# Performance work log

Measured on AMD Instinct MI355X. Metric: run time of the kernel, lower is better.

## Reference

```python
import jax, jax.numpy as jnp
import numpy as np
from math import sqrt

NUM_HEADS = 8
HIDDEN = 768
ATTN_DIM = HIDDEN // NUM_HEADS  # 96
NEG = -1e10


def setup_inputs() -> dict:
    key = jax.random.key(0)
    ks = jax.random.split(key, 6)
    b, s, dim = 8, 1024, 768
    scale = 1.0 / sqrt(dim)
    return {
        "span_embeddings": jax.random.normal(ks[0], (b, s, dim), dtype=jnp.float32),
        "span_tags": jax.random.randint(ks[1], (b, s), 0, 5),
        "w_weight": jax.random.normal(ks[2], (1, dim), dtype=jnp.float32) * scale,
        "w_q": jax.random.normal(ks[3], (HIDDEN, dim), dtype=jnp.float32) * scale,
        "w_k": jax.random.normal(ks[4], (HIDDEN, dim), dtype=jnp.float32) * scale,
        "w_v": jax.random.normal(ks[5], (HIDDEN, dim), dtype=jnp.float32) * scale,
    }


def reference(span_embeddings, span_tags, w_weight, w_q, w_k, w_v):
    b, s, _ = span_embeddings.shape
    pad = span_tags == 0  # [b, s]

    # additive span attention weights: Linear(dim -> 1), mask padded, softmax over seq
    attn_weights = span_embeddings @ w_weight.T  # [b, s, 1]
    attn_weights = jnp.where(pad[:, :, None], NEG, attn_weights)
    attn_weights = jax.nn.softmax(attn_weights, axis=1)

    # NOTE: original views hidden as (attn_dim, num_heads) in that order
    qs = (span_embeddings @ w_q.T).reshape(b, s, ATTN_DIM, NUM_HEADS)
    ks = (span_embeddings @ w_k.T).reshape(b, s, ATTN_DIM, NUM_HEADS)
    vs = (span_embeddings @ w_v.T).reshape(b, s, ATTN_DIM, NUM_HEADS)

    rel = jnp.einsum('bqdh,bkdh->bqkh', qs, ks) / sqrt(ATTN_DIM)  # [b,q,k,h]
    # original masks along query axis (relevance_weights[span_tags.eq(0)] = NEG)
    rel = jnp.where(pad[:, :, None, None], NEG, rel)
    # original softmax(dim=-1) -> over the HEADS axis (faithful quirk)
    rel = jax.nn.softmax(rel, axis=-1)

    span_value = jnp.einsum('bqkh,bkdh->bqdh', rel, vs).reshape(b, s, HIDDEN)
    weighted_value = jnp.sum(attn_weights * span_value, axis=1)  # [b, hidden]
    return weighted_value
```

## Files before the change

### kernel.cpp

```cpp
#include <hip/hip_runtime.h>
#include <hip/hip_bf16.h>
#include <math.h>

#define NEGV (-1e10f)

typedef __attribute__((ext_vector_type(8))) short bf16x8;
typedef __attribute__((ext_vector_type(4))) float f32x4;
typedef __attribute__((ext_vector_type(16))) float f32x16;

static __device__ __forceinline__ unsigned short f2bf(float f) {
  unsigned int u = __builtin_bit_cast(unsigned int, f);
  unsigned int r = (u + 0x7fffu + ((u >> 16) & 1u)) >> 16;
  return (unsigned short)r;
}
static __device__ __forceinline__ float bf2f(unsigned short v) {
  return __builtin_bit_cast(float, (unsigned int)v << 16);
}

#define GLD16(g, l)                                                   \
  __builtin_amdgcn_global_load_lds(                                   \
      (const __attribute__((address_space(1))) void*)(g),             \
      (__attribute__((address_space(3))) void*)(l), 16, 0, 0)

__global__ __launch_bounds__(256) void cast_inputs(
    const float* __restrict__ emb, const int* __restrict__ tags,
    const float* __restrict__ ww, const float* __restrict__ wq,
    const float* __restrict__ wk, const float* __restrict__ wv,
    unsigned short* __restrict__ embbf, float* __restrict__ logits,
    unsigned short* __restrict__ wbf) {
  int bx = blockIdx.x;
  if (bx < 2048) {
    int w = threadIdx.x >> 6, lane = threadIdx.x & 63;
    int row = bx * 4 + w;
    const float4* src = (const float4*)(emb + (size_t)row * 768);
    const float4* wsrc = (const float4*)ww;
    ushort4* dst = (ushort4*)(embbf + (size_t)row * 768);
    float d = 0.f;
#pragma unroll
    for (int j = 0; j < 3; j++) {
      int idx = lane + 64 * j;
      float4 v = src[idx];
      float4 wv = wsrc[idx];
      d += v.x * wv.x + v.y * wv.y + v.z * wv.z + v.w * wv.w;
      ushort4 o;
      o.x = f2bf(v.x); o.y = f2bf(v.y); o.z = f2bf(v.z); o.w = f2bf(v.w);
      dst[idx] = o;
    }
#pragma unroll
    for (int off = 32; off; off >>= 1) d += __shfl_xor(d, off);
    if (lane == 0) logits[row] = (tags[row] == 0) ? NEGV : d;
  } else {
    int g = bx - 2048;
    int z = g / 576;
    int idx = (g - z * 576) * 256 + threadIdx.x;
    const float* src = (z == 0) ? wq : (z == 1) ? wk : wv;
    float4 v = ((const float4*)src)[idx];
    ushort4 o;
    o.x = f2bf(v.x); o.y = f2bf(v.y); o.z = f2bf(v.z); o.w = f2bf(v.w);
    if (z == 2) {
      ((ushort4*)(wbf + (size_t)z * 589824))[idx] = o;
    } else {
      int f = idx / 192;
      int col4 = idx - f * 192;
      int h = f & 7, dg = f >> 3;
      int tt = dg >> 4, ddl = dg & 15;
      int wn = ddl >> 3, cb = (ddl >> 2) & 1, j = ddl & 3;
      int orow = tt * 128 + wn * 64 + j * 16 + cb * 8 + h;
      ((ushort4*)(wbf + (size_t)z * 589824))[orow * 192 + col4] = o;
    }
  }
}

__global__ __launch_bounds__(256) void softmax_aw(
    const float* __restrict__ logits, float* __restrict__ aw) {
  __shared__ float red[4];
  int b = blockIdx.x, t = threadIdx.x;
  const float* L = logits + b * 1024;
  float x0 = L[t], x1 = L[t + 256], x2 = L[t + 512], x3 = L[t + 768];
  float m = fmaxf(fmaxf(x0, x1), fmaxf(x2, x3));
#pragma unroll
  for (int off = 32; off; off >>= 1) m = fmaxf(m, __shfl_xor(m, off));
  if ((t & 63) == 0) red[t >> 6] = m;
  __syncthreads();
  m = fmaxf(fmaxf(red[0], red[1]), fmaxf(red[2], red[3]));
  float e0 = __expf(x0 - m), e1 = __expf(x1 - m), e2 = __expf(x2 - m),
        e3 = __expf(x3 - m);
  float s = e0 + e1 + e2 + e3;
#pragma unroll
  for (int off = 32; off; off >>= 1) s += __shfl_xor(s, off);
  __syncthreads();
  if ((t & 63) == 0) red[t >> 6] = s;
  __syncthreads();
  float inv = 1.0f / (red[0] + red[1] + red[2] + red[3]);
  float* A = aw + b * 1024;
  A[t] = e0 * inv; A[t + 256] = e1 * inv;
  A[t + 512] = e2 * inv; A[t + 768] = e3 * inv;
}

__global__ __launch_bounds__(256) void qkv_gemm(
    const unsigned short* __restrict__ A, const unsigned short* __restrict__ Wbf,
    unsigned short* __restrict__ Qf, unsigned short* __restrict__ Kf,
    unsigned short* __restrict__ Vbf) {
  __shared__ __align__(16) unsigned short sm[17408];
  unsigned short* As = sm;
  unsigned short* Bs = sm + 8192;
  int z = blockIdx.z;
  const unsigned short* B = Wbf + (size_t)z * 589824;
  int mb = blockIdx.x * 128, nb = blockIdx.y * 128;
  int tid = threadIdx.x;
  int w = tid >> 6, lane = tid & 63;
  int wm = w >> 1, wn = w & 1;
  int c = lane & 15, quad = lane >> 4;
  int lrow = lane >> 2;
  int lcol = ((lane & 3) ^ (lrow & 3)) * 8;
  const unsigned short* Ag = A + (size_t)(mb + w * 32 + lrow) * 768 + lcol;
  const unsigned short* Bg = B + (size_t)(nb + w * 32 + lrow) * 768 + lcol;
  int woff = w * 1024;

#define PREFETCH(buf, kb)                                              \
  do {                                                                 \
    GLD16(Ag + (kb), As + (buf) * 4096 + woff);                        \
    GLD16(Ag + (kb) + 16 * 768, As + (buf) * 4096 + woff + 512);       \
    GLD16(Bg + (kb), Bs + (buf) * 4096 + woff);                        \
    GLD16(Bg + (kb) + 16 * 768, Bs + (buf) * 4096 + woff + 512);       \
  } while (0)

  f32x4 acc[4][4];
#pragma unroll
  for (int i = 0; i < 4; i++)
#pragma unroll
    for (int j = 0; j < 4; j++) acc[i][j] = 0;

  PREFETCH(0, 0);
  for (int it = 0; it < 24; it++) {
    __syncthreads();
    if (it + 1 < 24) PREFETCH((it + 1) & 1, (it + 1) * 32);
    const unsigned short* Ab = As + (it & 1) * 4096;
    const unsigned short* Bb = Bs + (it & 1) * 4096;
    int sw = (quad ^ (c & 3)) * 8;
    bf16x8 af[4], bfr[4];
#pragma unroll
    for (int i = 0; i < 4; i++)
      af[i] = *(const bf16x8*)&Ab[(wm * 64 + i * 16 + c) * 32 + sw];
#pragma unroll
    for (int j = 0; j < 4; j++)
      bfr[j] = *(const bf16x8*)&Bb[(wn * 64 + j * 16 + c) * 32 + sw];
#pragma unroll
    for (int i = 0; i < 4; i++)
#pragma unroll
      for (int j = 0; j < 4; j++)
        acc[i][j] = __builtin_amdgcn_mfma_f32_16x16x32_bf16(af[i], bfr[j],
                                                            acc[i][j], 0, 0, 0);
  }
  __syncthreads();

  if (z == 2) {
#pragma unroll
    for (int i = 0; i < 4; i++)
#pragma unroll
      for (int j = 0; j < 4; j++)
#pragma unroll
        for (int r = 0; r < 4; r++) {
          int rl = wm * 64 + i * 16 + quad * 4 + r;
          int cl = wn * 64 + j * 16 + c;
          sm[rl * 136 + cl] = f2bf(acc[i][j][r]);
        }
    __syncthreads();
#pragma unroll
    for (int it2 = 0; it2 < 8; it2++) {
      int g2 = it2 * 256 + tid;
      int rl = g2 >> 4;
      int cu = (g2 & 15) * 8;
      bf16x8 vdat = *(const bf16x8*)&sm[rl * 136 + cu];
      *(bf16x8*)&Vbf[(size_t)(mb + rl) * 768 + nb + cu] = vdat;
    }
  } else {
    unsigned short* O = (z == 0) ? Qf : Kf;
#pragma unroll
    for (int i = 0; i < 4; i++) {
#pragma unroll
      for (int r = 0; r < 4; r++) {
        int qlr = wm * 64 + i * 16 + quad * 4 + r;
        int chunkL = (qlr >> 5) * 8 + (c & 7);
        int lane32 = (qlr & 31) + wn * 32;
        ushort4 pk;
        pk.x = f2bf(acc[i][0][r]);
        pk.y = f2bf(acc[i][1][r]);
        pk.z = f2bf(acc[i][2][r]);
        pk.w = f2bf(acc[i][3][r]);
        *(ushort4*)&sm[chunkL * 520 + lane32 * 8 + 4 * (c >> 3)] = pk;
      }
    }
    __syncthreads();
    int bq = mb >> 10;
    int qt32g0 = (mb & 1023) >> 5;
    int tt = blockIdx.y;
#pragma unroll
    for (int it2 = 0; it2 < 8; it2++) {
      int g = it2 * 256 + tid;
      int chunkL = g >> 6;
      int off = (g & 63) * 8;
      bf16x8 vdat = *(const bf16x8*)&sm[chunkL * 520 + off];
      int qt32 = qt32g0 + (chunkL >> 3), h = chunkL & 7;
      size_t dst = ((((size_t)(bq * 32 + qt32) * 8 + h) * 6 + tt) << 9) + off;
      *(bf16x8*)&O[dst] = vdat;
    }
  }
#undef PREFETCH
}

__global__ __launch_bounds__(256) void attn(
    const unsigned short* __restrict__ Qf, const unsigned short* __restrict__ Kf,
    const float* __restrict__ aw, float* __restrict__ Ptp) {
  __shared__ float pbuf[1024];
  int id = blockIdx.x;
  int b = id & 7, qb = (id >> 3) & 15, kb = id >> 7;
  int tid = threadIdx.x, w = tid >> 6, lane = tid & 63;
  int wq = w >> 1, wk = w & 1;
  const unsigned short* Qb =
      Qf + ((size_t)(b * 32 + qb * 2 + wq) * 48) * 512 + (size_t)lane * 8;
  const unsigned short* Kb =
      Kf + ((size_t)(b * 32 + kb * 2 + wk) * 48) * 512 + (size_t)lane * 8;

  f32x16 acc[8];
#pragma unroll
  for (int h = 0; h < 8; h++) acc[h] = 0;
#pragma unroll
  for (int h = 0; h < 8; h++) {
#pragma unroll
    for (int t = 0; t < 6; t++) {
      bf16x8 a = *(const bf16x8*)(Qb + (size_t)(h * 6 + t) * 512);
      bf16x8 bb = *(const bf16x8*)(Kb + (size_t)(h * 6 + t) * 512);
      acc[h] = __builtin_amdgcn_mfma_f32_32x32x16_bf16(a, bb, acc[h], 0, 0, 0);
    }
  }

  float awv[16];
#pragma unroll
  for (int reg = 0; reg < 16; reg++) {
    int row = (reg & 3) + 8 * (reg >> 2) + 4 * (lane >> 5);
    awv[reg] = aw[b * 1024 + qb * 64 + wq * 32 + row];
  }
  float partial[8];
#pragma unroll
  for (int h = 0; h < 8; h++) partial[h] = 0.f;
  const float C2 = 0.10206207261596577f * 1.4426950408889634f;
#pragma unroll
  for (int reg = 0; reg < 16; reg++) {
    float v[8];
    float ssum = 0.f;
#pragma unroll
    for (int h = 0; h < 8; h++) {
      float e = exp2f(acc[h][reg] * C2);
      v[h] = e;
      ssum += e;
    }
    float g = awv[reg] * __builtin_amdgcn_rcpf(ssum);
#pragma unroll
    for (int h = 0; h < 8; h++) partial[h] += v[h] * g;
  }
#pragma unroll
  for (int h = 0; h < 8; h++) {
    float v = partial[h];
    v += __shfl_xor(v, 32);
    partial[h] = v;
  }
  if (lane < 32) {
#pragma unroll
    for (int h = 0; h < 8; h++) pbuf[w * 256 + lane * 8 + h] = partial[h];
  }
  __syncthreads();
#pragma unroll
  for (int wk2 = 0; wk2 < 2; wk2++) {
    float s = pbuf[wk2 * 256 + tid] + pbuf[(2 + wk2) * 256 + tid];
    int kcol = tid >> 3, h = tid & 7;
    Ptp[(((size_t)qb * 8 + b) * 1024 + kb * 64 + wk2 * 32 + kcol) * 8 + h] = s;
  }
}

__global__ __launch_bounds__(256) void finalize(
    const float* __restrict__ Ptp, const unsigned short* __restrict__ Vbf,
    float* __restrict__ out) {
  __shared__ float ps[256];
  int kc = blockIdx.x, b = blockIdx.y;
  int t = threadIdx.x;
  {
    int k = kc * 32 + (t >> 3), h = t & 7;
    float s = 0.f;
#pragma unroll
    for (int qc = 0; qc < 16; qc++)
      s += Ptp[(((size_t)qc * 8 + b) * 1024 + k) * 8 + h];
    ps[t] = s;
  }
  __syncthreads();
  if (t < 192) {
    int o0 = t * 4;
    int hb = o0 & 7;
    float a0 = 0, a1 = 0, a2 = 0, a3 = 0;
    const unsigned short* Vb = Vbf + ((size_t)b * 1024 + kc * 32) * 768 + o0;
#pragma unroll 4
    for (int kk = 0; kk < 32; kk++) {
      ushort4 vv = *(const ushort4*)(Vb + (size_t)kk * 768);
      const float* p = &ps[kk * 8 + hb];
      a0 += p[0] * bf2f(vv.x);
      a1 += p[1] * bf2f(vv.y);
      a2 += p[2] * bf2f(vv.z);
      a3 += p[3] * bf2f(vv.w);
    }
    atomicAdd(&out[b * 768 + o0], a0);
    atomicAdd(&out[b * 768 + o0 + 1], a1);
    atomicAdd(&out[b * 768 + o0 + 2], a2);
    atomicAdd(&out[b * 768 + o0 + 3], a3);
  }
}

extern "C" void kernel_launch(void* const* d_in, const int* in_sizes, int n_in,
                              void* d_out, int out_size, void* d_ws,
                              size_t ws_size, hipStream_t stream) {
  const float* emb = (const float*)d_in[0];
  const int* tags = (const int*)d_in[1];
  const float* ww = (const float*)d_in[2];
  const float* wq = (const float*)d_in[3];
  const float* wk = (const float*)d_in[4];
  const float* wv = (const float*)d_in[5];
  float* out = (float*)d_out;
  char* ws = (char*)d_ws;
  unsigned short* embbf = (unsigned short*)(ws + 0);
  unsigned short* wbf   = (unsigned short*)(ws + 12582912);
  unsigned short* Qf    = (unsigned short*)(ws + 16121856);
  unsigned short* Kf    = (unsigned short*)(ws + 28704768);
  unsigned short* Vbf   = (unsigned short*)(ws + 41287680);
  float* logits         = (float*)(ws + 53870592);
  float* aw             = (float*)(ws + 53903360);
  float* Ptp            = (float*)(ws + 53936128);

  hipMemsetAsync(out, 0, 8 * 768 * sizeof(float), stream);
  cast_inputs<<<3776, 256, 0, stream>>>(emb, tags, ww, wq, wk, wv, embbf,
                                        logits, wbf);
  softmax_aw<<<8, 256, 0, stream>>>(logits, aw);
  qkv_gemm<<<dim3(64, 6, 3), 256, 0, stream>>>(embbf, wbf, Qf, Kf, Vbf);
  attn<<<2048, 256, 0, stream>>>(Qf, Kf, aw, Ptp);
  finalize<<<dim3(32, 8), 256, 0, stream>>>(Ptp, Vbf, out);
}
```

Measured before the change: 171.1 us.

## Pre-swizzle GEMM operands into MFMA fragment layout and drop LDS staging

The cast kernel now writes the bf16 embeddings and weights directly in a per-lane MFMA fragment layout (16-row by 32-column chunks of 512 elements). The QKV GEMM then loads fragments straight from global memory into registers, with no LDS double buffering and no per-iteration barriers. The cast kernel is reorganized to 384 threads per block and uses a shared-memory atomic reduction for the attention logits. The trade-off is that each wave re-reads operands from global or L2 memory instead of sharing them through LDS. Global loads also have longer latency than LDS reads, and only loop unrolling is left to hide it.

```diff
diff --git a/kernel.cpp b/kernel.cpp
--- a/kernel.cpp
+++ b/kernel.cpp
@@ -17,57 +17,66 @@
   return __builtin_bit_cast(float, (unsigned int)v << 16);
 }
 
-#define GLD16(g, l)                                                   \
-  __builtin_amdgcn_global_load_lds(                                   \
-      (const __attribute__((address_space(1))) void*)(g),             \
-      (__attribute__((address_space(3))) void*)(l), 16, 0, 0)
-
-__global__ __launch_bounds__(256) void cast_inputs(
+
+__global__ __launch_bounds__(384) void cast_inputs(
     const float* __restrict__ emb, const int* __restrict__ tags,
     const float* __restrict__ ww, const float* __restrict__ wq,
     const float* __restrict__ wk, const float* __restrict__ wv,
-    unsigned short* __restrict__ embbf, float* __restrict__ logits,
-    unsigned short* __restrict__ wbf) {
-  int bx = blockIdx.x;
+    unsigned short* __restrict__ Af, float* __restrict__ logits,
+    unsigned short* __restrict__ Wf) {
+  __shared__ float lred[4];
+  int bx = blockIdx.x, t = threadIdx.x;
   if (bx < 2048) {
-    int w = threadIdx.x >> 6, lane = threadIdx.x & 63;
-    int row = bx * 4 + w;
-    const float4* src = (const float4*)(emb + (size_t)row * 768);
-    const float4* wsrc = (const float4*)ww;
-    ushort4* dst = (ushort4*)(embbf + (size_t)row * 768);
-    float d = 0.f;
-#pragma unroll
-    for (int j = 0; j < 3; j++) {
-      int idx = lane + 64 * j;
-      float4 v = src[idx];
-      float4 wv = wsrc[idx];
-      d += v.x * wv.x + v.y * wv.y + v.z * wv.z + v.w * wv.w;
-      ushort4 o;
-      o.x = f2bf(v.x); o.y = f2bf(v.y); o.z = f2bf(v.z); o.w = f2bf(v.w);
-      dst[idx] = o;
-    }
-#pragma unroll
-    for (int off = 32; off; off >>= 1) d += __shfl_xor(d, off);
-    if (lane == 0) logits[row] = (tags[row] == 0) ? NEGV : d;
+    int row = bx * 4 + t / 96;
+    int seg = t % 96, k0 = seg * 8;
+    if (t < 4) lred[t] = 0.f;
+    __syncthreads();
+    const float4* p = (const float4*)(emb + (size_t)row * 768 + k0);
+    const float4* wp = (const float4*)(ww + k0);
+    float4 v0 = p[0], v1 = p[1];
+    float4 w0 = wp[0], w1 = wp[1];
+    float d = v0.x * w0.x + v0.y * w0.y + v0.z * w0.z + v0.w * w0.w +
+              v1.x * w1.x + v1.y * w1.y + v1.z * w1.z + v1.w * w1.w;
+    atomicAdd(&lred[t / 96], d);
+    int chunk = (row >> 4) * 24 + (k0 >> 5);
+    int lane32 = (row & 15) + 16 * ((k0 >> 3) & 3);
+    ushort4 o0, o1;
+    o0.x = f2bf(v0.x); o0.y = f2bf(v0.y); o0.z = f2bf(v0.z); o0.w = f2bf(v0.w);
+    o1.x = f2bf(v1.x); o1.y = f2bf(v1.y); o1.z = f2bf(v1.z); o1.w = f2bf(v1.w);
+    ushort4* dst = (ushort4*)(Af + (size_t)chunk * 512 + lane32 * 8);
+    dst[0] = o0;
+    dst[1] = o1;
+    __syncthreads();
+    if (t < 4) {
+      int r = bx * 4 + t;
+      logits[r] = (tags[r] == 0) ? NEGV : lred[t];
+    }
   } else {
-    int g = bx - 2048;
-    int z = g / 576;
-    int idx = (g - z * 576) * 256 + threadIdx.x;
+    int g = (bx - 2048) * 384 + t;
+    int z = g / 73728;
+    int rem = g - z * 73728;
+    int f = rem / 96, seg = rem % 96, k0 = seg * 8;
     const float* src = (z == 0) ? wq : (z == 1) ? wk : wv;
-    float4 v = ((const float4*)src)[idx];
-    ushort4 o;
-    o.x = f2bf(v.x); o.y = f2bf(v.y); o.z = f2bf(v.z); o.w = f2bf(v.w);
+    const float4* p = (const float4*)(src + (size_t)f * 768 + k0);
+    float4 v0 = p[0], v1 = p[1];
+    int orow;
     if (z == 2) {
-      ((ushort4*)(wbf + (size_t)z * 589824))[idx] = o;
+      orow = f;
     } else {
-      int f = idx / 192;
-      int col4 = idx - f * 192;
       int h = f & 7, dg = f >> 3;
       int tt = dg >> 4, ddl = dg & 15;
       int wn = ddl >> 3, cb = (ddl >> 2) & 1, j = ddl & 3;
-      int orow = tt * 128 + wn * 64 + j * 16 + cb * 8 + h;
-      ((ushort4*)(wbf + (size_t)z * 589824))[orow * 192 + col4] = o;
-    }
+      orow = tt * 128 + wn * 64 + j * 16 + cb * 8 + h;
+    }
+    int chunk = (orow >> 4) * 24 + (k0 >> 5);
+    int lane32 = (orow & 15) + 16 * ((k0 >> 3) & 3);
+    ushort4 o0, o1;
+    o0.x = f2bf(v0.x); o0.y = f2bf(v0.y); o0.z = f2bf(v0.z); o0.w = f2bf(v0.w);
+    o1.x = f2bf(v1.x); o1.y = f2bf(v1.y); o1.z = f2bf(v1.z); o1.w = f2bf(v1.w);
+    ushort4* dst =
+        (ushort4*)(Wf + (size_t)z * 589824 + (size_t)chunk * 512 + lane32 * 8);
+    dst[0] = o0;
+    dst[1] = o1;
   }
 }
 
@@ -98,32 +107,21 @@
 }
 
 __global__ __launch_bounds__(256) void qkv_gemm(
-    const unsigned short* __restrict__ A, const unsigned short* __restrict__ Wbf,
+    const unsigned short* __restrict__ Af, const unsigned short* __restrict__ Wf,
     unsigned short* __restrict__ Qf, unsigned short* __restrict__ Kf,
     unsigned short* __restrict__ Vbf) {
   __shared__ __align__(16) unsigned short sm[17408];
-  unsigned short* As = sm;
-  unsigned short* Bs = sm + 8192;
   int z = blockIdx.z;
-  const unsigned short* B = Wbf + (size_t)z * 589824;
   int mb = blockIdx.x * 128, nb = blockIdx.y * 128;
   int tid = threadIdx.x;
   int w = tid >> 6, lane = tid & 63;
   int wm = w >> 1, wn = w & 1;
   int c = lane & 15, quad = lane >> 4;
-  int lrow = lane >> 2;
-  int lcol = ((lane & 3) ^ (lrow & 3)) * 8;
-  const unsigned short* Ag = A + (size_t)(mb + w * 32 + lrow) * 768 + lcol;
-  const unsigned short* Bg = B + (size_t)(nb + w * 32 + lrow) * 768 + lcol;
-  int woff = w * 1024;
-
-#define PREFETCH(buf, kb)                                              \
-  do {                                                                 \
-    GLD16(Ag + (kb), As + (buf) * 4096 + woff);                        \
-    GLD16(Ag + (kb) + 16 * 768, As + (buf) * 4096 + woff + 512);       \
-    GLD16(Bg + (kb), Bs + (buf) * 4096 + woff);                        \
-    GLD16(Bg + (kb) + 16 * 768, Bs + (buf) * 4096 + woff + 512);       \
-  } while (0)
+  const unsigned short* Ab =
+      Af + ((size_t)((mb >> 4) + wm * 4) * 24) * 512 + (size_t)lane * 8;
+  const unsigned short* Bb = Wf + (size_t)z * 589824 +
+                             ((size_t)((nb >> 4) + wn * 4) * 24) * 512 +
+                             (size_t)lane * 8;
 
   f32x4 acc[4][4];
 #pragma unroll
@@ -131,20 +129,15 @@
 #pragma unroll
     for (int j = 0; j < 4; j++) acc[i][j] = 0;
 
-  PREFETCH(0, 0);
+#pragma unroll 4
   for (int it = 0; it < 24; it++) {
-    __syncthreads();
-    if (it + 1 < 24) PREFETCH((it + 1) & 1, (it + 1) * 32);
-    const unsigned short* Ab = As + (it & 1) * 4096;
-    const unsigned short* Bb = Bs + (it & 1) * 4096;
-    int sw = (quad ^ (c & 3)) * 8;
     bf16x8 af[4], bfr[4];
 #pragma unroll
     for (int i = 0; i < 4; i++)
-      af[i] = *(const bf16x8*)&Ab[(wm * 64 + i * 16 + c) * 32 + sw];
+      af[i] = *(const bf16x8*)(Ab + (size_t)(i * 24 + it) * 512);
 #pragma unroll
     for (int j = 0; j < 4; j++)
-      bfr[j] = *(const bf16x8*)&Bb[(wn * 64 + j * 16 + c) * 32 + sw];
+      bfr[j] = *(const bf16x8*)(Bb + (size_t)(j * 24 + it) * 512);
 #pragma unroll
     for (int i = 0; i < 4; i++)
 #pragma unroll
@@ -152,7 +145,6 @@
         acc[i][j] = __builtin_amdgcn_mfma_f32_16x16x32_bf16(af[i], bfr[j],
                                                             acc[i][j], 0, 0, 0);
   }
-  __syncthreads();
 
   if (z == 2) {
 #pragma unroll
@@ -206,7 +198,6 @@
       *(bf16x8*)&O[dst] = vdat;
     }
   }
-#undef PREFETCH
 }
 
 __global__ __launch_bounds__(256) void attn(
@@ -325,20 +316,20 @@
   const float* wv = (const float*)d_in[5];
   float* out = (float*)d_out;
   char* ws = (char*)d_ws;
-  unsigned short* embbf = (unsigned short*)(ws + 0);
-  unsigned short* wbf   = (unsigned short*)(ws + 12582912);
-  unsigned short* Qf    = (unsigned short*)(ws + 16121856);
-  unsigned short* Kf    = (unsigned short*)(ws + 28704768);
-  unsigned short* Vbf   = (unsigned short*)(ws + 41287680);
-  float* logits         = (float*)(ws + 53870592);
-  float* aw             = (float*)(ws + 53903360);
-  float* Ptp            = (float*)(ws + 53936128);
+  unsigned short* Af  = (unsigned short*)(ws + 0);
+  unsigned short* Wf  = (unsigned short*)(ws + 12582912);
+  unsigned short* Qf  = (unsigned short*)(ws + 16121856);
+  unsigned short* Kf  = (unsigned short*)(ws + 28704768);
+  unsigned short* Vbf = (unsigned short*)(ws + 41287680);
+  float* logits       = (float*)(ws + 53870592);
+  float* aw           = (float*)(ws + 53903360);
+  float* Ptp          = (float*)(ws + 53936128);
 
   hipMemsetAsync(out, 0, 8 * 768 * sizeof(float), stream);
-  cast_inputs<<<3776, 256, 0, stream>>>(emb, tags, ww, wq, wk, wv, embbf,
-                                        logits, wbf);
+  cast_inputs<<<2624, 384, 0, stream>>>(emb, tags, ww, wq, wk, wv, Af, logits,
+                                        Wf);
   softmax_aw<<<8, 256, 0, stream>>>(logits, aw);
-  qkv_gemm<<<dim3(64, 6, 3), 256, 0, stream>>>(embbf, wbf, Qf, Kf, Vbf);
+  qkv_gemm<<<dim3(64, 6, 3), 256, 0, stream>>>(Af, Wf, Qf, Kf, Vbf);
   attn<<<2048, 256, 0, stream>>>(Qf, Kf, aw, Ptp);
   finalize<<<dim3(32, 8), 256, 0, stream>>>(Ptp, Vbf, out);
 }
```

After: 179.5 us. 4.9% more time.

## Split attn heads across waves with LDS softmax sum exchange; fold output zeroing

Applied to the files above, without the earlier changes.

The attn kernel now assigns each wave half the heads (4 instead of 8) with one 32-query tile per block, so each wave keeps fewer accumulators. Per-row exponent sums are exchanged between the paired waves through LDS to finish the softmax over all 8 heads, and launch bounds request 4 blocks per SIMD for higher occupancy. The grid doubles, and finalize now sums 32 query-chunk partials instead of 16. The output memset is folded into softmax_aw, and Ptp reuses the embedding buffer region, which is safe only because qkv_gemm runs before attn.

```diff
diff --git a/kernel.cpp b/kernel.cpp
--- a/kernel.cpp
+++ b/kernel.cpp
@@ -72,9 +72,13 @@
 }
 
 __global__ __launch_bounds__(256) void softmax_aw(
-    const float* __restrict__ logits, float* __restrict__ aw) {
+    const float* __restrict__ logits, float* __restrict__ aw,
+    float* __restrict__ out) {
   __shared__ float red[4];
   int b = blockIdx.x, t = threadIdx.x;
+  out[b * 768 + t] = 0.f;
+  out[b * 768 + t + 256] = 0.f;
+  out[b * 768 + t + 512] = 0.f;
   const float* L = logits + b * 1024;
   float x0 = L[t], x1 = L[t + 256], x2 = L[t + 512], x3 = L[t + 768];
   float m = fmaxf(fmaxf(x0, x1), fmaxf(x2, x3));
@@ -209,72 +213,69 @@
 #undef PREFETCH
 }
 
-__global__ __launch_bounds__(256) void attn(
+__global__ __launch_bounds__(256, 4) void attn(
     const unsigned short* __restrict__ Qf, const unsigned short* __restrict__ Kf,
     const float* __restrict__ aw, float* __restrict__ Ptp) {
-  __shared__ float pbuf[1024];
+  __shared__ float ex[4 * 1024];
   int id = blockIdx.x;
-  int b = id & 7, qb = (id >> 3) & 15, kb = id >> 7;
+  int b = id & 7, qb = (id >> 3) & 31, kb = id >> 8;
   int tid = threadIdx.x, w = tid >> 6, lane = tid & 63;
-  int wq = w >> 1, wk = w & 1;
+  int hh = w & 1, wk = w >> 1;
   const unsigned short* Qb =
-      Qf + ((size_t)(b * 32 + qb * 2 + wq) * 48) * 512 + (size_t)lane * 8;
+      Qf + ((size_t)((b * 32 + qb) * 8 + hh * 4) * 6) * 512 + (size_t)lane * 8;
   const unsigned short* Kb =
-      Kf + ((size_t)(b * 32 + kb * 2 + wk) * 48) * 512 + (size_t)lane * 8;
-
-  f32x16 acc[8];
-#pragma unroll
-  for (int h = 0; h < 8; h++) acc[h] = 0;
-#pragma unroll
-  for (int h = 0; h < 8; h++) {
+      Kf + ((size_t)((b * 32 + kb * 2 + wk) * 8 + hh * 4) * 6) * 512 +
+      (size_t)lane * 8;
+
+  f32x16 acc[4];
+#pragma unroll
+  for (int hi = 0; hi < 4; hi++) acc[hi] = 0;
+#pragma unroll
+  for (int hi = 0; hi < 4; hi++) {
 #pragma unroll
     for (int t = 0; t < 6; t++) {
-      bf16x8 a = *(const bf16x8*)(Qb + (size_t)(h * 6 + t) * 512);
-      bf16x8 bb = *(const bf16x8*)(Kb + (size_t)(h * 6 + t) * 512);
-      acc[h] = __builtin_amdgcn_mfma_f32_32x32x16_bf16(a, bb, acc[h], 0, 0, 0);
-    }
-  }
-
-  float awv[16];
+      bf16x8 a = *(const bf16x8*)(Qb + (size_t)(hi * 6 + t) * 512);
+      bf16x8 bb = *(const bf16x8*)(Kb + (size_t)(hi * 6 + t) * 512);
+      acc[hi] = __builtin_amdgcn_mfma_f32_32x32x16_bf16(a, bb, acc[hi], 0, 0, 0);
+    }
+  }
+
+  const float C2 = 0.10206207261596577f * 1.4426950408889634f;
+  float esum[16];
 #pragma unroll
   for (int reg = 0; reg < 16; reg++) {
-    int row = (reg & 3) + 8 * (reg >> 2) + 4 * (lane >> 5);
-    awv[reg] = aw[b * 1024 + qb * 64 + wq * 32 + row];
-  }
-  float partial[8];
-#pragma unroll
-  for (int h = 0; h < 8; h++) partial[h] = 0.f;
-  const float C2 = 0.10206207261596577f * 1.4426950408889634f;
+    float s = 0.f;
+#pragma unroll
+    for (int hi = 0; hi < 4; hi++) {
+      float e = exp2f(acc[hi][reg] * C2);
+      acc[hi][reg] = e;
+      s += e;
+    }
+    esum[reg] = s;
+    ex[w * 1024 + reg * 64 + lane] = s;
+  }
+  __syncthreads();
+  const float* exP = &ex[(w ^ 1) * 1024];
+  float partial[4];
+#pragma unroll
+  for (int hi = 0; hi < 4; hi++) partial[hi] = 0.f;
 #pragma unroll
   for (int reg = 0; reg < 16; reg++) {
-    float v[8];
-    float ssum = 0.f;
-#pragma unroll
-    for (int h = 0; h < 8; h++) {
-      float e = exp2f(acc[h][reg] * C2);
-      v[h] = e;
-      ssum += e;
-    }
-    float g = awv[reg] * __builtin_amdgcn_rcpf(ssum);
-#pragma unroll
-    for (int h = 0; h < 8; h++) partial[h] += v[h] * g;
-  }
-#pragma unroll
-  for (int h = 0; h < 8; h++) {
-    float v = partial[h];
-    v += __shfl_xor(v, 32);
-    partial[h] = v;
-  }
+    float tot = esum[reg] + exP[reg * 64 + lane];
+    int rowq = (reg & 3) + 8 * (reg >> 2) + 4 * (lane >> 5);
+    float awv = aw[b * 1024 + qb * 32 + rowq];
+    float g = awv * __builtin_amdgcn_rcpf(tot);
+#pragma unroll
+    for (int hi = 0; hi < 4; hi++) partial[hi] += acc[hi][reg] * g;
+  }
+#pragma unroll
+  for (int hi = 0; hi < 4; hi++) partial[hi] += __shfl_xor(partial[hi], 32);
   if (lane < 32) {
-#pragma unroll
-    for (int h = 0; h < 8; h++) pbuf[w * 256 + lane * 8 + h] = partial[h];
-  }
-  __syncthreads();
-#pragma unroll
-  for (int wk2 = 0; wk2 < 2; wk2++) {
-    float s = pbuf[wk2 * 256 + tid] + pbuf[(2 + wk2) * 256 + tid];
-    int kcol = tid >> 3, h = tid & 7;
-    Ptp[(((size_t)qb * 8 + b) * 1024 + kb * 64 + wk2 * 32 + kcol) * 8 + h] = s;
+    f32x4 o;
+    o[0] = partial[0]; o[1] = partial[1];
+    o[2] = partial[2]; o[3] = partial[3];
+    *(f32x4*)&Ptp[(((size_t)qb * 8 + b) * 1024 + kb * 64 + wk * 32 + lane) * 8 +
+                  hh * 4] = o;
   }
 }
 
@@ -288,7 +289,7 @@
     int k = kc * 32 + (t >> 3), h = t & 7;
     float s = 0.f;
 #pragma unroll
-    for (int qc = 0; qc < 16; qc++)
+    for (int qc = 0; qc < 32; qc++)
       s += Ptp[(((size_t)qc * 8 + b) * 1024 + k) * 8 + h];
     ps[t] = s;
   }
@@ -326,19 +327,18 @@
   float* out = (float*)d_out;
   char* ws = (char*)d_ws;
   unsigned short* embbf = (unsigned short*)(ws + 0);
+  float* Ptp            = (float*)(ws + 0);
   unsigned short* wbf   = (unsigned short*)(ws + 12582912);
   unsigned short* Qf    = (unsigned short*)(ws + 16121856);
   unsigned short* Kf    = (unsigned short*)(ws + 28704768);
   unsigned short* Vbf   = (unsigned short*)(ws + 41287680);
   float* logits         = (float*)(ws + 53870592);
   float* aw             = (float*)(ws + 53903360);
-  float* Ptp            = (float*)(ws + 53936128);
-
-  hipMemsetAsync(out, 0, 8 * 768 * sizeof(float), stream);
+
   cast_inputs<<<3776, 256, 0, stream>>>(emb, tags, ww, wq, wk, wv, embbf,
                                         logits, wbf);
-  softmax_aw<<<8, 256, 0, stream>>>(logits, aw);
+  softmax_aw<<<8, 256, 0, stream>>>(logits, aw, out);
   qkv_gemm<<<dim3(64, 6, 3), 256, 0, stream>>>(embbf, wbf, Qf, Kf, Vbf);
-  attn<<<2048, 256, 0, stream>>>(Qf, Kf, aw, Ptp);
+  attn<<<4096, 256, 0, stream>>>(Qf, Kf, aw, Ptp);
   finalize<<<dim3(32, 8), 256, 0, stream>>>(Ptp, Vbf, out);
 }
```

Measured after the change: 176.6 us. +3.2%, slower.

## Reassociate V projection after attention contraction to drop V GEMM

Applied to the files above, without the earlier changes.

Instead of projecting all tokens through Wv and then contracting with attention probabilities, the probabilities are first contracted with bf16 embeddings per head (rcomp), then the small per-head result is multiplied by fp32 Wv (vproj). This removes a third of the QKV GEMM, the Wv cast, the V buffer write/read and the output atomics/memset. It adds two small kernels, with vproj using only 8 blocks that each stream the full Wv matrix, which may be latency bound.

```diff
diff --git a/kernel.cpp b/kernel.cpp
--- a/kernel.cpp
+++ b/kernel.cpp
@@ -25,9 +25,8 @@
 __global__ __launch_bounds__(256) void cast_inputs(
     const float* __restrict__ emb, const int* __restrict__ tags,
     const float* __restrict__ ww, const float* __restrict__ wq,
-    const float* __restrict__ wk, const float* __restrict__ wv,
-    unsigned short* __restrict__ embbf, float* __restrict__ logits,
-    unsigned short* __restrict__ wbf) {
+    const float* __restrict__ wk, unsigned short* __restrict__ embbf,
+    float* __restrict__ logits, unsigned short* __restrict__ wbf) {
   int bx = blockIdx.x;
   if (bx < 2048) {
     int w = threadIdx.x >> 6, lane = threadIdx.x & 63;
@@ -53,21 +52,17 @@
     int g = bx - 2048;
     int z = g / 576;
     int idx = (g - z * 576) * 256 + threadIdx.x;
-    const float* src = (z == 0) ? wq : (z == 1) ? wk : wv;
+    const float* src = (z == 0) ? wq : wk;
     float4 v = ((const float4*)src)[idx];
     ushort4 o;
     o.x = f2bf(v.x); o.y = f2bf(v.y); o.z = f2bf(v.z); o.w = f2bf(v.w);
-    if (z == 2) {
-      ((ushort4*)(wbf + (size_t)z * 589824))[idx] = o;
-    } else {
-      int f = idx / 192;
-      int col4 = idx - f * 192;
-      int h = f & 7, dg = f >> 3;
-      int tt = dg >> 4, ddl = dg & 15;
-      int wn = ddl >> 3, cb = (ddl >> 2) & 1, j = ddl & 3;
-      int orow = tt * 128 + wn * 64 + j * 16 + cb * 8 + h;
-      ((ushort4*)(wbf + (size_t)z * 589824))[orow * 192 + col4] = o;
-    }
+    int f = idx / 192;
+    int col4 = idx - f * 192;
+    int h = f & 7, dg = f >> 3;
+    int tt = dg >> 4, ddl = dg & 15;
+    int wn = ddl >> 3, cb = (ddl >> 2) & 1, j = ddl & 3;
+    int orow = tt * 128 + wn * 64 + j * 16 + cb * 8 + h;
+    ((ushort4*)(wbf + (size_t)z * 589824))[orow * 192 + col4] = o;
   }
 }
 
@@ -99,8 +94,7 @@
 
 __global__ __launch_bounds__(256) void qkv_gemm(
     const unsigned short* __restrict__ A, const unsigned short* __restrict__ Wbf,
-    unsigned short* __restrict__ Qf, unsigned short* __restrict__ Kf,
-    unsigned short* __restrict__ Vbf) {
+    unsigned short* __restrict__ Qf, unsigned short* __restrict__ Kf) {
   __shared__ __align__(16) unsigned short sm[17408];
   unsigned short* As = sm;
   unsigned short* Bs = sm + 8192;
@@ -154,57 +148,35 @@
   }
   __syncthreads();
 
-  if (z == 2) {
-#pragma unroll
-    for (int i = 0; i < 4; i++)
-#pragma unroll
-      for (int j = 0; j < 4; j++)
-#pragma unroll
-        for (int r = 0; r < 4; r++) {
-          int rl = wm * 64 + i * 16 + quad * 4 + r;
-          int cl = wn * 64 + j * 16 + c;
-          sm[rl * 136 + cl] = f2bf(acc[i][j][r]);
-        }
-    __syncthreads();
-#pragma unroll
-    for (int it2 = 0; it2 < 8; it2++) {
-      int g2 = it2 * 256 + tid;
-      int rl = g2 >> 4;
-      int cu = (g2 & 15) * 8;
-      bf16x8 vdat = *(const bf16x8*)&sm[rl * 136 + cu];
-      *(bf16x8*)&Vbf[(size_t)(mb + rl) * 768 + nb + cu] = vdat;
-    }
-  } else {
-    unsigned short* O = (z == 0) ? Qf : Kf;
-#pragma unroll
-    for (int i = 0; i < 4; i++) {
-#pragma unroll
-      for (int r = 0; r < 4; r++) {
-        int qlr = wm * 64 + i * 16 + quad * 4 + r;
-        int chunkL = (qlr >> 5) * 8 + (c & 7);
-        int lane32 = (qlr & 31) + wn * 32;
-        ushort4 pk;
-        pk.x = f2bf(acc[i][0][r]);
-        pk.y = f2bf(acc[i][1][r]);
-        pk.z = f2bf(acc[i][2][r]);
-        pk.w = f2bf(acc[i][3][r]);
-        *(ushort4*)&sm[chunkL * 520 + lane32 * 8 + 4 * (c >> 3)] = pk;
-      }
-    }
-    __syncthreads();
-    int bq = mb >> 10;
-    int qt32g0 = (mb & 1023) >> 5;
-    int tt = blockIdx.y;
-#pragma unroll
-    for (int it2 = 0; it2 < 8; it2++) {
-      int g = it2 * 256 + tid;
-      int chunkL = g >> 6;
-      int off = (g & 63) * 8;
-      bf16x8 vdat = *(const bf16x8*)&sm[chunkL * 520 + off];
-      int qt32 = qt32g0 + (chunkL >> 3), h = chunkL & 7;
-      size_t dst = ((((size_t)(bq * 32 + qt32) * 8 + h) * 6 + tt) << 9) + off;
-      *(bf16x8*)&O[dst] = vdat;
-    }
+  unsigned short* O = (z == 0) ? Qf : Kf;
+#pragma unroll
+  for (int i = 0; i < 4; i++) {
+#pragma unroll
+    for (int r = 0; r < 4; r++) {
+      int qlr = wm * 64 + i * 16 + quad * 4 + r;
+      int chunkL = (qlr >> 5) * 8 + (c & 7);
+      int lane32 = (qlr & 31) + wn * 32;
+      ushort4 pk;
+      pk.x = f2bf(acc[i][0][r]);
+      pk.y = f2bf(acc[i][1][r]);
+      pk.z = f2bf(acc[i][2][r]);
+      pk.w = f2bf(acc[i][3][r]);
+      *(ushort4*)&sm[chunkL * 520 + lane32 * 8 + 4 * (c >> 3)] = pk;
+    }
+  }
+  __syncthreads();
+  int bq = mb >> 10;
+  int qt32g0 = (mb & 1023) >> 5;
+  int tt = blockIdx.y;
+#pragma unroll
+  for (int it2 = 0; it2 < 8; it2++) {
+    int g = it2 * 256 + tid;
+    int chunkL = g >> 6;
+    int off = (g & 63) * 8;
+    bf16x8 vdat = *(const bf16x8*)&sm[chunkL * 520 + off];
+    int qt32 = qt32g0 + (chunkL >> 3), h = chunkL & 7;
+    size_t dst = ((((size_t)(bq * 32 + qt32) * 8 + h) * 6 + tt) << 9) + off;
+    *(bf16x8*)&O[dst] = vdat;
   }
 #undef PREFETCH
 }
@@ -278,40 +250,80 @@
   }
 }
 
-__global__ __launch_bounds__(256) void finalize(
-    const float* __restrict__ Ptp, const unsigned short* __restrict__ Vbf,
-    float* __restrict__ out) {
-  __shared__ float ps[256];
+__global__ __launch_bounds__(192) void rcomp(
+    const float* __restrict__ Ptp, const unsigned short* __restrict__ embbf,
+    float* __restrict__ Rp) {
+  __shared__ float pbk[64 * 8];
   int kc = blockIdx.x, b = blockIdx.y;
   int t = threadIdx.x;
-  {
-    int k = kc * 32 + (t >> 3), h = t & 7;
+  if (t < 64) {
+    int k = kc * 64 + t;
+    f32x4 s0 = 0, s1 = 0;
+#pragma unroll
+    for (int qc = 0; qc < 16; qc++) {
+      const float* p = &Ptp[(((size_t)qc * 8 + b) * 1024 + k) * 8];
+      s0 += *(const f32x4*)p;
+      s1 += *(const f32x4*)(p + 4);
+    }
+    *(f32x4*)&pbk[t * 8] = s0;
+    *(f32x4*)&pbk[t * 8 + 4] = s1;
+  }
+  __syncthreads();
+  int d0 = t * 4;
+  float acc[8][4];
+#pragma unroll
+  for (int h = 0; h < 8; h++)
+#pragma unroll
+    for (int j = 0; j < 4; j++) acc[h][j] = 0.f;
+  const unsigned short* eb =
+      embbf + ((size_t)(b * 1024 + kc * 64)) * 768 + d0;
+#pragma unroll 4
+  for (int k = 0; k < 64; k++) {
+    ushort4 ev = *(const ushort4*)(eb + (size_t)k * 768);
+    float e0 = bf2f(ev.x), e1 = bf2f(ev.y), e2 = bf2f(ev.z), e3 = bf2f(ev.w);
+    const float* pr = &pbk[k * 8];
+#pragma unroll
+    for (int h = 0; h < 8; h++) {
+      float p = pr[h];
+      acc[h][0] += p * e0;
+      acc[h][1] += p * e1;
+      acc[h][2] += p * e2;
+      acc[h][3] += p * e3;
+    }
+  }
+#pragma unroll
+  for (int h = 0; h < 8; h++) {
+    f32x4 o;
+    o[0] = acc[h][0]; o[1] = acc[h][1]; o[2] = acc[h][2]; o[3] = acc[h][3];
+    *(f32x4*)&Rp[(((size_t)kc * 8 + b) * 8 + h) * 768 + d0] = o;
+  }
+}
+
+__global__ __launch_bounds__(768) void vproj(
+    const float* __restrict__ Rp, const float* __restrict__ wv,
+    float* __restrict__ out) {
+  __shared__ float Rs[8 * 772];
+  int b = blockIdx.x, t = threadIdx.x;
+#pragma unroll
+  for (int i = 0; i < 8; i++) {
     float s = 0.f;
 #pragma unroll
-    for (int qc = 0; qc < 16; qc++)
-      s += Ptp[(((size_t)qc * 8 + b) * 1024 + k) * 8 + h];
-    ps[t] = s;
-  }
-  __syncthreads();
-  if (t < 192) {
-    int o0 = t * 4;
-    int hb = o0 & 7;
-    float a0 = 0, a1 = 0, a2 = 0, a3 = 0;
-    const unsigned short* Vb = Vbf + ((size_t)b * 1024 + kc * 32) * 768 + o0;
+    for (int kc = 0; kc < 16; kc++)
+      s += Rp[(((size_t)kc * 8 + b) * 8 + i) * 768 + t];
+    Rs[i * 772 + t] = s;
+  }
+  __syncthreads();
+  int h = t & 7;
+  const float4* wr = (const float4*)(wv + (size_t)t * 768);
+  const float* rr = &Rs[h * 772];
+  float a = 0.f;
 #pragma unroll 4
-    for (int kk = 0; kk < 32; kk++) {
-      ushort4 vv = *(const ushort4*)(Vb + (size_t)kk * 768);
-      const float* p = &ps[kk * 8 + hb];
-      a0 += p[0] * bf2f(vv.x);
-      a1 += p[1] * bf2f(vv.y);
-      a2 += p[2] * bf2f(vv.z);
-      a3 += p[3] * bf2f(vv.w);
-    }
-    atomicAdd(&out[b * 768 + o0], a0);
-    atomicAdd(&out[b * 768 + o0 + 1], a1);
-    atomicAdd(&out[b * 768 + o0 + 2], a2);
-    atomicAdd(&out[b * 768 + o0 + 3], a3);
-  }
+  for (int d4 = 0; d4 < 192; d4++) {
+    float4 wvv = wr[d4];
+    const float* r = rr + d4 * 4;
+    a += wvv.x * r[0] + wvv.y * r[1] + wvv.z * r[2] + wvv.w * r[3];
+  }
+  out[b * 768 + t] = a;
 }
 
 extern "C" void kernel_launch(void* const* d_in, const int* in_sizes, int n_in,
@@ -329,16 +341,16 @@
   unsigned short* wbf   = (unsigned short*)(ws + 12582912);
   unsigned short* Qf    = (unsigned short*)(ws + 16121856);
   unsigned short* Kf    = (unsigned short*)(ws + 28704768);
-  unsigned short* Vbf   = (unsigned short*)(ws + 41287680);
   float* logits         = (float*)(ws + 53870592);
   float* aw             = (float*)(ws + 53903360);
   float* Ptp            = (float*)(ws + 53936128);
-
-  hipMemsetAsync(out, 0, 8 * 768 * sizeof(float), stream);
-  cast_inputs<<<3776, 256, 0, stream>>>(emb, tags, ww, wq, wk, wv, embbf,
-                                        logits, wbf);
+  float* Rp             = (float*)(ws + 58130432);
+
+  cast_inputs<<<3200, 256, 0, stream>>>(emb, tags, ww, wq, wk, embbf, logits,
+                                        wbf);
   softmax_aw<<<8, 256, 0, stream>>>(logits, aw);
-  qkv_gemm<<<dim3(64, 6, 3), 256, 0, stream>>>(embbf, wbf, Qf, Kf, Vbf);
+  qkv_gemm<<<dim3(64, 6, 2), 256, 0, stream>>>(embbf, wbf, Qf, Kf);
   attn<<<2048, 256, 0, stream>>>(Qf, Kf, aw, Ptp);
-  finalize<<<dim3(32, 8), 256, 0, stream>>>(Ptp, Vbf, out);
-}
+  rcomp<<<dim3(16, 8), 192, 0, stream>>>(Ptp, embbf, Rp);
+  vproj<<<8, 768, 0, stream>>>(Rp, wv, out);
+}
```

After: 253.8 us. +48.3%, slower.
